# Kernel tuning notes

Hardware: AMD Instinct MI355X
Metric: run time of the kernel (lower is better)

Reference implementation:

```python
import jax, jax.numpy as jnp
import numpy as np
from jax import lax

DROP_PROB = 0.1
BLOCK_SIZE = 7
B, C, H, W = 64, 256, 56, 56
HM, WM = H - (BLOCK_SIZE - 1), W - (BLOCK_SIZE - 1)


def setup_inputs() -> dict:
    key = jax.random.key(0)
    k1, k2 = jax.random.split(key)
    x = jax.random.normal(k1, (B, C, H, W), dtype=jnp.float32)
    mask_u = jax.random.uniform(k2, (B, C, HM, WM), dtype=jnp.float32)
    return {"x": x, "mask_u": mask_u}


def reference(x, mask_u):
    bs = BLOCK_SIZE
    feat = x.shape[2]
    # gamma as in _compute_gamma
    gamma = DROP_PROB / bs**2 * feat**2 / (feat - bs + 1) ** 2
    # Bernoulli(gamma) sample, deterministic given mask_u
    mask = (mask_u < gamma).astype(x.dtype)  # (B,C,HM,WM)
    # The nonzero/scatter block expansion in the original is exactly a
    # stride-1 max-pool with a bs x bs window and (bs-1, bs-1) zero padding,
    # producing the (B,C,H,W) padded dropped-region mask.
    blocked = lax.reduce_window(
        mask, 0.0, lax.max,
        window_dimensions=(1, 1, bs, bs),
        window_strides=(1, 1, 1, 1),
        padding=((0, 0), (0, 0), (bs - 1, bs - 1), (bs - 1, bs - 1)),
    )
    block_mask = 1.0 - blocked  # (B,C,H,W)
    scale = block_mask.size / block_mask.sum()
    return x * block_mask * scale
```

## Files before the change

### kernel.cpp

```cpp
#include <hip/hip_runtime.h>


#define BB 64
#define CC 256
#define HH 56
#define WW 56
#define HMM 50
#define WMM 50
#define BS 7

static constexpr unsigned int NPLANE = BB * CC;
static constexpr unsigned int NTOT   = BB * CC * HH * WW;
static constexpr unsigned int NV     = NTOT / 4;

__global__ void __launch_bounds__(64) dropblock_mask_kernel(
    const float* __restrict__ mask_u,
    unsigned long long* __restrict__ rowmask,
    unsigned int* __restrict__ plane_cnt,
    float gamma)
{
    const unsigned int plane = blockIdx.x;
    const unsigned int lane  = threadIdx.x;
    const float* mu = mask_u + (size_t)plane * (HMM * WMM);

    __shared__ unsigned long long rsh[HMM];

    #pragma unroll 5
    for (int i = 0; i < HMM; ++i) {
        float v = (lane < WMM) ? mu[i * WMM + lane] : 1.0f;
        unsigned long long m = __ballot(v < gamma);
        unsigned long long d = m | (m << 1);
        d |= d << 2;
        d |= d << 3;
        if (lane == 0) rsh[i] = d;
    }
    __syncthreads();

    unsigned long long blocked = 0ull;
    if (lane < HH) {
        int lo = (int)lane - (BS - 1); if (lo < 0) lo = 0;
        int hi = (int)lane;            if (hi > HMM - 1) hi = HMM - 1;
        for (int di = lo; di <= hi; ++di) blocked |= rsh[di];
        rowmask[plane * HH + lane] = blocked;
    }

    unsigned int cnt = __popcll(blocked);
    #pragma unroll
    for (int off = 32; off > 0; off >>= 1)
        cnt += __shfl_down(cnt, off, 64);
    if (lane == 0) plane_cnt[plane] = cnt;
}

__global__ void __launch_bounds__(1024) dropblock_scale_kernel(
    const unsigned int* __restrict__ plane_cnt,
    float* __restrict__ scale_out)
{
    __shared__ unsigned int ssum[16];
    const unsigned int t = threadIdx.x;

    const uint4* pc4 = reinterpret_cast<const uint4*>(plane_cnt);
    uint4 a = pc4[t];
    uint4 b = pc4[t + 1024];
    uint4 c = pc4[t + 2048];
    uint4 d = pc4[t + 3072];
    unsigned int s = a.x + a.y + a.z + a.w
                   + b.x + b.y + b.z + b.w
                   + c.x + c.y + c.z + c.w
                   + d.x + d.y + d.z + d.w;

    #pragma unroll
    for (int off = 32; off > 0; off >>= 1)
        s += __shfl_down(s, off, 64);
    if ((t & 63u) == 0u) ssum[t >> 6] = s;
    __syncthreads();

    if (t < 16) {
        unsigned int v = ssum[t];
        #pragma unroll
        for (int off = 8; off > 0; off >>= 1)
            v += __shfl_down(v, off, 64);
        if (t == 0) {
            *scale_out = (float)NTOT / (float)(NTOT - v);
        }
    }
}

__global__ void __launch_bounds__(256) dropblock_apply_kernel(
    const float* __restrict__ x,
    const unsigned long long* __restrict__ rowmask,
    const float* __restrict__ scale_ptr,
    float* __restrict__ out)
{
    unsigned int idx = blockIdx.x * 256u + threadIdx.x;
    if (idx >= NV) return;

    const float scale = *scale_ptr;

    unsigned int plane = idx / (HH * WW / 4);
    unsigned int rem   = idx - plane * (HH * WW / 4);
    unsigned int row   = rem / (WW / 4);
    unsigned int colv  = rem - row * (WW / 4);
    unsigned int col   = colv * 4;

    unsigned long long rm = rowmask[plane * HH + row];
    float4 xv = reinterpret_cast<const float4*>(x)[idx];
    float4 o;
    o.x = ((rm >> (col + 0)) & 1ull) ? 0.0f : xv.x * scale;
    o.y = ((rm >> (col + 1)) & 1ull) ? 0.0f : xv.y * scale;
    o.z = ((rm >> (col + 2)) & 1ull) ? 0.0f : xv.z * scale;
    o.w = ((rm >> (col + 3)) & 1ull) ? 0.0f : xv.w * scale;
    reinterpret_cast<float4*>(out)[idx] = o;
}

extern "C" void kernel_launch(void* const* d_in, const int* in_sizes, int n_in,
                              void* d_out, int out_size, void* d_ws, size_t ws_size,
                              hipStream_t stream) {
    const float* x      = (const float*)d_in[0];
    const float* mask_u = (const float*)d_in[1];
    float* out          = (float*)d_out;

    float* scale_ws             = (float*)d_ws;
    unsigned int* plane_cnt     = (unsigned int*)((char*)d_ws + 64);
    unsigned long long* rowmask = (unsigned long long*)((char*)d_ws + 65600);

    const double gd = 0.1 / ((double)BS * BS) * ((double)HH * HH) /
                      (((double)HH - BS + 1.0) * ((double)HH - BS + 1.0));
    const float gamma = (float)gd;

    dropblock_mask_kernel<<<NPLANE, 64, 0, stream>>>(mask_u, rowmask, plane_cnt, gamma);

    dropblock_scale_kernel<<<1, 1024, 0, stream>>>(plane_cnt, scale_ws);

    dropblock_apply_kernel<<<(NV + 255u) / 256u, 256, 0, stream>>>(
        x, rowmask, scale_ws, out);
}
```

Baseline: 455.5 us.

## Pack four planes per mask block and widen apply kernel with nontemporal accesses

The mask kernel now runs four wavefronts per block, one plane each. It keeps each row's dilated bits in a register and does the vertical OR with shuffles instead of shared memory and a barrier, which cuts launch overhead and the shared-memory round trip. The apply kernel handles 8 floats per thread, reads an 8-bit slice of the row mask, and uses nontemporal loads and stores so the 200MB stream bypasses cache pollution. Removing the bounds check depends on NP being an exact multiple of 256.

```diff
diff --git a/kernel.cpp b/kernel.cpp
--- a/kernel.cpp
+++ b/kernel.cpp
@@ -12,37 +12,39 @@
 static constexpr unsigned int NPLANE = BB * CC;
 static constexpr unsigned int NTOT   = BB * CC * HH * WW;
 static constexpr unsigned int NV     = NTOT / 4;
+static constexpr unsigned int NP     = NV / 2;
 
-__global__ void __launch_bounds__(64) dropblock_mask_kernel(
+typedef float f32x4 __attribute__((ext_vector_type(4)));
+
+__global__ void __launch_bounds__(256) dropblock_mask_kernel(
     const float* __restrict__ mask_u,
     unsigned long long* __restrict__ rowmask,
     unsigned int* __restrict__ plane_cnt,
     float gamma)
 {
-    const unsigned int plane = blockIdx.x;
-    const unsigned int lane  = threadIdx.x;
+    const unsigned int wid   = threadIdx.x >> 6;
+    const unsigned int lane  = threadIdx.x & 63u;
+    const unsigned int plane = blockIdx.x * 4u + wid;
     const float* mu = mask_u + (size_t)plane * (HMM * WMM);
 
-    __shared__ unsigned long long rsh[HMM];
+    unsigned long long my_d = 0ull;
 
-    #pragma unroll 5
+    #pragma unroll
     for (int i = 0; i < HMM; ++i) {
         float v = (lane < WMM) ? mu[i * WMM + lane] : 1.0f;
         unsigned long long m = __ballot(v < gamma);
         unsigned long long d = m | (m << 1);
         d |= d << 2;
         d |= d << 3;
-        if (lane == 0) rsh[i] = d;
+        if (lane == (unsigned)i) my_d = d;
     }
-    __syncthreads();
 
-    unsigned long long blocked = 0ull;
-    if (lane < HH) {
-        int lo = (int)lane - (BS - 1); if (lo < 0) lo = 0;
-        int hi = (int)lane;            if (hi > HMM - 1) hi = HMM - 1;
-        for (int di = lo; di <= hi; ++di) blocked |= rsh[di];
-        rowmask[plane * HH + lane] = blocked;
-    }
+    unsigned long long blocked = my_d;
+    blocked |= __shfl_up(blocked, 1, 64);
+    blocked |= __shfl_up(blocked, 2, 64);
+    blocked |= __shfl_up(blocked, 3, 64);
+
+    if (lane < HH) rowmask[plane * HH + lane] = blocked;
 
     unsigned int cnt = __popcll(blocked);
     #pragma unroll
@@ -91,25 +93,32 @@
     const float* __restrict__ scale_ptr,
     float* __restrict__ out)
 {
-    unsigned int idx = blockIdx.x * 256u + threadIdx.x;
-    if (idx >= NV) return;
-
+    const unsigned int p = blockIdx.x * 256u + threadIdx.x;
     const float scale = *scale_ptr;
 
-    unsigned int plane = idx / (HH * WW / 4);
-    unsigned int rem   = idx - plane * (HH * WW / 4);
-    unsigned int row   = rem / (WW / 4);
-    unsigned int colv  = rem - row * (WW / 4);
-    unsigned int col   = colv * 4;
+    unsigned int plane = p / 392u;
+    unsigned int rem   = p - plane * 392u;
+    unsigned int row   = rem / 7u;
+    unsigned int pc    = rem - row * 7u;
 
-    unsigned long long rm = rowmask[plane * HH + row];
-    float4 xv = reinterpret_cast<const float4*>(x)[idx];
-    float4 o;
-    o.x = ((rm >> (col + 0)) & 1ull) ? 0.0f : xv.x * scale;
-    o.y = ((rm >> (col + 1)) & 1ull) ? 0.0f : xv.y * scale;
-    o.z = ((rm >> (col + 2)) & 1ull) ? 0.0f : xv.z * scale;
-    o.w = ((rm >> (col + 3)) & 1ull) ? 0.0f : xv.w * scale;
-    reinterpret_cast<float4*>(out)[idx] = o;
+    unsigned int rbits =
+        (unsigned int)(rowmask[plane * HH + row] >> (pc * 8u)) & 0xffu;
+
+    const f32x4* xp = reinterpret_cast<const f32x4*>(x) + (size_t)p * 2u;
+    f32x4 a = __builtin_nontemporal_load(xp);
+    f32x4 b = __builtin_nontemporal_load(xp + 1);
+
+    f32x4 oa, ob;
+    #pragma unroll
+    for (int j = 0; j < 4; ++j)
+        oa[j] = ((rbits >> j) & 1u) ? 0.0f : a[j] * scale;
+    #pragma unroll
+    for (int j = 0; j < 4; ++j)
+        ob[j] = ((rbits >> (4 + j)) & 1u) ? 0.0f : b[j] * scale;
+
+    f32x4* op = reinterpret_cast<f32x4*>(out) + (size_t)p * 2u;
+    __builtin_nontemporal_store(oa, op);
+    __builtin_nontemporal_store(ob, op + 1);
 }
 
 extern "C" void kernel_launch(void* const* d_in, const int* in_sizes, int n_in,
@@ -127,10 +136,11 @@
                       (((double)HH - BS + 1.0) * ((double)HH - BS + 1.0));
     const float gamma = (float)gd;
 
-    dropblock_mask_kernel<<<NPLANE, 64, 0, stream>>>(mask_u, rowmask, plane_cnt, gamma);
+    dropblock_mask_kernel<<<NPLANE / 4, 256, 0, stream>>>(
+        mask_u, rowmask, plane_cnt, gamma);
 
     dropblock_scale_kernel<<<1, 1024, 0, stream>>>(plane_cnt, scale_ws);
 
-    dropblock_apply_kernel<<<(NV + 255u) / 256u, 256, 0, stream>>>(
+    dropblock_apply_kernel<<<NP / 256u, 256, 0, stream>>>(
         x, rowmask, scale_ws, out);
 }
```

After: 464.5 us. No clear change (+2.0%).
